# Kernel optimization log

Hardware: AMD Instinct MI355X
Metric: run time of the kernel (lower is better)

The kernel has to match this reference:

```python
import jax, jax.numpy as jnp
import numpy as np

E, D_IN, D_OUT = 8, 1024, 1024
B, S = 4, 2048

def setup_inputs() -> dict:
    key = jax.random.key(0)
    k_x, k_g, k_gb, k_w = jax.random.split(key, 4)
    x = jax.random.normal(k_x, (B, S, D_IN), dtype=jnp.float32)
    gate_w = jax.random.normal(k_g, (D_IN, E), dtype=jnp.float32) * 0.02
    gate_b = jax.random.normal(k_gb, (E,), dtype=jnp.float32) * 0.02
    expert_w = jax.random.normal(k_w, (E, D_IN, D_OUT), dtype=jnp.float32) * 0.02
    return {"x": x, "gate_w": gate_w, "gate_b": gate_b, "expert_w": expert_w}

def reference(x, gate_w, gate_b, expert_w):
    # gate: softmax over experts
    gate_score = jax.nn.softmax(x @ gate_w + gate_b, axis=-1)        # [B,S,E]
    # all-expert dense GEMM: [B,S,E,out]
    expert_out = jnp.einsum('bsi,eio->bseo', x, expert_w)
    # gate-weighted combine: [B,S,out]
    out = jnp.einsum('bse,bseo->bso', gate_score, expert_out)
    return out
```

## Files before the change

### kernel.cpp

```cpp
#include <hip/hip_runtime.h>
#include <hip/hip_bf16.h>
#include <cstdint>

#define TOKENS 8192
#define DIN 1024
#define DOUT 1024
#define NE 8

typedef __bf16 bf16;
typedef __attribute__((ext_vector_type(8))) __bf16 bf16x8;
typedef __attribute__((ext_vector_type(4))) float floatx4;
typedef __attribute__((ext_vector_type(2))) float floatx2;

__device__ __forceinline__ void async16(const void* gptr, void* lptr) {
  __builtin_amdgcn_global_load_lds(
      (const __attribute__((address_space(1))) void*)gptr,
      (__attribute__((address_space(3))) void*)lptr,
      16, 0, 0);
}

__global__ __launch_bounds__(256) void gate_kernel(
    const float* __restrict__ x, const float* __restrict__ gw,
    const float* __restrict__ gb, float* __restrict__ g,
    bf16* __restrict__ xbf) {
  __shared__ __align__(16) float gws[NE * DIN];
  __shared__ __align__(16) bf16 xtile[8][1032];

  const int tid = threadIdx.x;
  const int bg = blockIdx.x;
#pragma unroll
  for (int k = 0; k < 8; ++k) {
    const int base = (k * 256 + tid) * 4;
    const floatx4 v = *(const floatx4*)(gw + base);
#pragma unroll
    for (int m = 0; m < 4; ++m) {
      const int j = base + m;
      gws[(j & 7) * DIN + (j >> 3)] = v[m];
    }
  }
  __syncthreads();

  const int lane = tid & 63;
  const int wave = tid >> 6;

#pragma unroll
  for (int h = 0; h < 2; ++h) {
#pragma unroll
    for (int tt = 0; tt < 2; ++tt) {
      const int tl = h * 8 + tt * 4 + wave;
      const int t = bg * 16 + tl;
      const float* xr = x + (size_t)t * DIN;
      bf16* const xrow = &xtile[tl & 7][0];

      float acc[NE];
#pragma unroll
      for (int e = 0; e < NE; ++e) acc[e] = 0.f;

#pragma unroll
      for (int it = 0; it < 4; ++it) {
        const int i = it * 256 + lane * 4;
        const floatx4 xv = *(const floatx4*)(xr + i);
        union { bf16 b[4]; uint64_t u; } cv;
#pragma unroll
        for (int m = 0; m < 4; ++m) cv.b[m] = (bf16)xv[m];
        *(uint64_t*)(xrow + i) = cv.u;
#pragma unroll
        for (int e = 0; e < NE; ++e) {
          const floatx4 wv = *(const floatx4*)(gws + e * DIN + i);
          acc[e] += xv[0] * wv[0] + xv[1] * wv[1] + xv[2] * wv[2] + xv[3] * wv[3];
        }
      }
#pragma unroll
      for (int e = 0; e < NE; ++e)
#pragma unroll
        for (int off = 32; off > 0; off >>= 1)
          acc[e] += __shfl_xor(acc[e], off, 64);

      float lg[NE];
      float mx = -3.0e38f;
#pragma unroll
      for (int e = 0; e < NE; ++e) { lg[e] = acc[e] + gb[e]; mx = fmaxf(mx, lg[e]); }
      float s = 0.f;
#pragma unroll
      for (int e = 0; e < NE; ++e) { lg[e] = __expf(lg[e] - mx); s += lg[e]; }
      const float inv = 1.f / s;
      if (lane == 0) {
        floatx4 o0, o1;
#pragma unroll
        for (int e = 0; e < 4; ++e) { o0[e] = lg[e] * inv; o1[e] = lg[e + 4] * inv; }
        *(floatx4*)(g + (size_t)t * NE) = o0;
        *(floatx4*)(g + (size_t)t * NE + 4) = o1;
      }
    }
    __syncthreads();
#pragma unroll
    for (int p = 0; p < 4; ++p) {
      const int u = p * 256 + tid;
      const int lr3 = u & 7;
      const int lq = (u >> 3) & 3;
      const int kkv = (u >> 5) & 1;
      const int kt = u >> 6;
      const bf16x8 v = *(const bf16x8*)(&xtile[lr3][kt * 64 + kkv * 32 + lq * 8]);
      const size_t off = (size_t)bg * 16384 +
          (size_t)((((kt * 2 + kkv) * 4 + lq) * 16) + h * 8 + lr3) * 8;
      *(bf16x8*)(xbf + off) = v;
    }
    __syncthreads();
  }
}

__global__ __launch_bounds__(256) void trans_kernel(
    const float* __restrict__ w, bf16* __restrict__ wt) {
  __shared__ __align__(16) float tile[64][65];
  const int b = blockIdx.x;
  const int e = b >> 8;
  const int i0 = ((b >> 4) & 15) * 64;
  const int o0 = (b & 15) * 64;
  const int tid = threadIdx.x;
  const int c4 = (tid & 15) * 4;
  const int r = tid >> 4;

  const float* src = w + ((size_t)e * DIN + i0) * DOUT + o0;
#pragma unroll
  for (int rr = r; rr < 64; rr += 16) {
    const floatx4 v = *(const floatx4*)(src + (size_t)rr * DOUT + c4);
    tile[rr][c4] = v[0]; tile[rr][c4 + 1] = v[1];
    tile[rr][c4 + 2] = v[2]; tile[rr][c4 + 3] = v[3];
  }
  __syncthreads();
  bf16* dst = wt + ((size_t)e * DOUT + o0) * DIN + i0;
#pragma unroll
  for (int rr = r; rr < 64; rr += 16) {
    union { bf16 b[4]; uint64_t u; } cv;
#pragma unroll
    for (int j = 0; j < 4; ++j) cv.b[j] = (bf16)tile[c4 + j][rr];
    *(uint64_t*)(dst + (size_t)rr * DIN + c4) = cv.u;
  }
}

__global__ __launch_bounds__(256, 2) void moe_gemm(
    const bf16* __restrict__ xbf, const bf16* __restrict__ wt,
    const float* __restrict__ g, float* __restrict__ out) {
  __shared__ __align__(16) bf16 Bs[2][128 * 64];

  const int tid = threadIdx.x;
  const int c = blockIdx.x & 7;
  const int jj = blockIdx.x >> 3;
  const int bm = (c >> 1) * 16 + (jj & 15);
  const int bn = (c & 1) * 4 + (jj >> 4);
  const int lane = tid & 63;
  const int wave = tid >> 6;
  const int wm = wave >> 1, wn = wave & 1;
  const int lr = lane & 15, lq = lane >> 4;

  const int srow = tid >> 3;
  const int scol = (((tid & 7) ^ (srow & 7)) << 3);
  const int kx = lr & 7;

  const bf16* const bgp = wt + (size_t)(bn * 128 + srow) * DIN + scol;
  const bf16* const abase = xbf + (size_t)(bm * 8 + wm * 4) * 16384 + lane * 8;

  const floatx4 fzero = {0.f, 0.f, 0.f, 0.f};
  floatx4 accF[4][4], accE[4][4];
#pragma unroll
  for (int im = 0; im < 4; ++im)
#pragma unroll
    for (int in = 0; in < 4; ++in) { accF[im][in] = fzero; accE[im][in] = fzero; }

  const int tok0 = bm * 128 + wm * 64;

  {
    bf16* const blp = &Bs[0][tid * 8];
#pragma unroll
    for (int j = 0; j < 4; ++j)
      async16(bgp + (size_t)(32 * j) * DIN, blp + j * 2048);
  }
  bf16x8 avc[2][4], avn[2][4];
#pragma unroll
  for (int kk = 0; kk < 2; ++kk)
#pragma unroll
    for (int im = 0; im < 4; ++im)
      avc[kk][im] = *(const bf16x8*)(abase + (size_t)im * 16384 + kk * 512);
  __syncthreads();

  for (int t = 0; t < 128; ++t) {
    const bf16* const Bb = &Bs[t & 1][0];

    bf16x8 bv[2][4];
#pragma unroll
    for (int kk = 0; kk < 2; ++kk) {
      const int kg = ((kk * 4 + lq) ^ kx) << 3;
#pragma unroll
      for (int in = 0; in < 4; ++in)
        bv[kk][in] = *(const bf16x8*)(Bb + (wn * 64 + in * 16 + lr) * 64 + kg);
    }

    const int t1 = t + 1;
    if (t1 < 128) {
      const int kt1 = t1 & 15;
#pragma unroll
      for (int kk = 0; kk < 2; ++kk)
#pragma unroll
        for (int im = 0; im < 4; ++im)
          avn[kk][im] = *(const bf16x8*)(abase + (size_t)im * 16384 +
                                         (kt1 * 2 + kk) * 512);
      const bf16* const bsrc = bgp + ((size_t)(t1 >> 4) << 20) + (size_t)kt1 * 64;
      bf16* const blp = &Bs[t1 & 1][tid * 8];
#pragma unroll
      for (int j = 0; j < 4; ++j)
        async16(bsrc + (size_t)(32 * j) * DIN, blp + j * 2048);
    }

    __builtin_amdgcn_s_setprio(1);
#pragma unroll
    for (int im = 0; im < 4; ++im)
#pragma unroll
      for (int in = 0; in < 4; ++in)
        accE[im][in] = __builtin_amdgcn_mfma_f32_16x16x32_bf16(
            avc[0][im], bv[0][in], accE[im][in], 0, 0, 0);
    __builtin_amdgcn_s_setprio(0);

    __builtin_amdgcn_s_setprio(1);
#pragma unroll
    for (int im = 0; im < 4; ++im)
#pragma unroll
      for (int in = 0; in < 4; ++in)
        accE[im][in] = __builtin_amdgcn_mfma_f32_16x16x32_bf16(
            avc[1][im], bv[1][in], accE[im][in], 0, 0, 0);
    __builtin_amdgcn_s_setprio(0);

    if ((t & 15) == 15) {
      const int e = t >> 4;
#pragma unroll
      for (int im = 0; im < 4; ++im) {
        float gv[4];
#pragma unroll
        for (int r = 0; r < 4; ++r)
          gv[r] = g[(size_t)(tok0 + im * 16 + lq * 4 + r) * NE + e];
#pragma unroll
        for (int in = 0; in < 4; ++in)
#pragma unroll
          for (int r = 0; r < 4; ++r) {
            accF[im][in][r] += gv[r] * accE[im][in][r];
            accE[im][in][r] = 0.f;
          }
      }
    }

    __syncthreads();

#pragma unroll
    for (int kk = 0; kk < 2; ++kk)
#pragma unroll
      for (int im = 0; im < 4; ++im)
        avc[kk][im] = avn[kk][im];
  }

#pragma unroll
  for (int im = 0; im < 4; ++im)
#pragma unroll
    for (int in = 0; in < 4; ++in) {
      const int col = bn * 128 + wn * 64 + in * 16 + lr;
#pragma unroll
      for (int r = 0; r < 4; ++r)
        out[(size_t)(tok0 + im * 16 + lq * 4 + r) * DOUT + col] =
            accF[im][in][r];
    }
}

extern "C" void kernel_launch(void* const* d_in, const int* in_sizes, int n_in,
                              void* d_out, int out_size, void* d_ws,
                              size_t ws_size, hipStream_t stream) {
  const float* x  = (const float*)d_in[0];
  const float* gw = (const float*)d_in[1];
  const float* gb = (const float*)d_in[2];
  const float* w  = (const float*)d_in[3];
  float* out = (float*)d_out;

  char* ws = (char*)d_ws;
  float* g   = (float*)ws;
  bf16* xbf  = (bf16*)(ws + 262144);
  bf16* wt   = (bf16*)(ws + 262144 + (size_t)TOKENS * DIN * 2);

  trans_kernel<<<2048, 256, 0, stream>>>(w, wt);
  gate_kernel<<<512, 256, 0, stream>>>(x, gw, gb, g, xbf);
  moe_gemm<<<512, 256, 0, stream>>>(xbf, wt, g, out);
}
```

Baseline: 242.1 us.

## Merge prep kernels and deepen GEMM B-tile pipeline to four LDS stages

```diff
diff --git a/kernel.cpp b/kernel.cpp
--- a/kernel.cpp
+++ b/kernel.cpp
@@ -10,7 +10,6 @@
 typedef __bf16 bf16;
 typedef __attribute__((ext_vector_type(8))) __bf16 bf16x8;
 typedef __attribute__((ext_vector_type(4))) float floatx4;
-typedef __attribute__((ext_vector_type(2))) float floatx2;
 
 __device__ __forceinline__ void async16(const void* gptr, void* lptr) {
   __builtin_amdgcn_global_load_lds(
@@ -19,129 +18,201 @@
       16, 0, 0);
 }
 
-__global__ __launch_bounds__(256) void gate_kernel(
+__global__ __launch_bounds__(256) void prep_kernel(
     const float* __restrict__ x, const float* __restrict__ gw,
     const float* __restrict__ gb, float* __restrict__ g,
-    bf16* __restrict__ xbf) {
-  __shared__ __align__(16) float gws[NE * DIN];
+    bf16* __restrict__ xbf, const float* __restrict__ w,
+    bf16* __restrict__ wt) {
+  __shared__ __align__(16) float smem[NE * DIN];
   __shared__ __align__(16) bf16 xtile[8][1032];
 
   const int tid = threadIdx.x;
-  const int bg = blockIdx.x;
-#pragma unroll
-  for (int k = 0; k < 8; ++k) {
-    const int base = (k * 256 + tid) * 4;
-    const floatx4 v = *(const floatx4*)(gw + base);
-#pragma unroll
-    for (int m = 0; m < 4; ++m) {
-      const int j = base + m;
-      gws[(j & 7) * DIN + (j >> 3)] = v[m];
-    }
-  }
-  __syncthreads();
-
-  const int lane = tid & 63;
-  const int wave = tid >> 6;
-
-#pragma unroll
-  for (int h = 0; h < 2; ++h) {
-#pragma unroll
-    for (int tt = 0; tt < 2; ++tt) {
-      const int tl = h * 8 + tt * 4 + wave;
-      const int t = bg * 16 + tl;
-      const float* xr = x + (size_t)t * DIN;
-      bf16* const xrow = &xtile[tl & 7][0];
-
-      float acc[NE];
-#pragma unroll
-      for (int e = 0; e < NE; ++e) acc[e] = 0.f;
-
-#pragma unroll
-      for (int it = 0; it < 4; ++it) {
-        const int i = it * 256 + lane * 4;
-        const floatx4 xv = *(const floatx4*)(xr + i);
-        union { bf16 b[4]; uint64_t u; } cv;
-#pragma unroll
-        for (int m = 0; m < 4; ++m) cv.b[m] = (bf16)xv[m];
-        *(uint64_t*)(xrow + i) = cv.u;
-#pragma unroll
-        for (int e = 0; e < NE; ++e) {
-          const floatx4 wv = *(const floatx4*)(gws + e * DIN + i);
-          acc[e] += xv[0] * wv[0] + xv[1] * wv[1] + xv[2] * wv[2] + xv[3] * wv[3];
+  if (blockIdx.x < 512) {
+    const int bg = blockIdx.x;
+#pragma unroll
+    for (int k = 0; k < 8; ++k) {
+      const int base = (k * 256 + tid) * 4;
+      const floatx4 v = *(const floatx4*)(gw + base);
+#pragma unroll
+      for (int m = 0; m < 4; ++m) {
+        const int j = base + m;
+        smem[(j & 7) * DIN + (j >> 3)] = v[m];
+      }
+    }
+    __syncthreads();
+
+    const int lane = tid & 63;
+    const int wave = tid >> 6;
+
+#pragma unroll
+    for (int h = 0; h < 2; ++h) {
+#pragma unroll
+      for (int tt = 0; tt < 2; ++tt) {
+        const int tl = h * 8 + tt * 4 + wave;
+        const int t = bg * 16 + tl;
+        const float* xr = x + (size_t)t * DIN;
+        bf16* const xrow = &xtile[tl & 7][0];
+
+        float acc[NE];
+#pragma unroll
+        for (int e = 0; e < NE; ++e) acc[e] = 0.f;
+
+#pragma unroll
+        for (int it = 0; it < 4; ++it) {
+          const int i = it * 256 + lane * 4;
+          const floatx4 xv = *(const floatx4*)(xr + i);
+          union { bf16 b[4]; uint64_t u; } cv;
+#pragma unroll
+          for (int m = 0; m < 4; ++m) cv.b[m] = (bf16)xv[m];
+          *(uint64_t*)(xrow + i) = cv.u;
+#pragma unroll
+          for (int e = 0; e < NE; ++e) {
+            const floatx4 wv = *(const floatx4*)(smem + e * DIN + i);
+            acc[e] += xv[0] * wv[0] + xv[1] * wv[1] + xv[2] * wv[2] + xv[3] * wv[3];
+          }
+        }
+#pragma unroll
+        for (int e = 0; e < NE; ++e)
+#pragma unroll
+          for (int off = 32; off > 0; off >>= 1)
+            acc[e] += __shfl_xor(acc[e], off, 64);
+
+        float lg[NE];
+        float mx = -3.0e38f;
+#pragma unroll
+        for (int e = 0; e < NE; ++e) { lg[e] = acc[e] + gb[e]; mx = fmaxf(mx, lg[e]); }
+        float s = 0.f;
+#pragma unroll
+        for (int e = 0; e < NE; ++e) { lg[e] = __expf(lg[e] - mx); s += lg[e]; }
+        const float inv = 1.f / s;
+        if (lane == 0) {
+          floatx4 o0, o1;
+#pragma unroll
+          for (int e = 0; e < 4; ++e) { o0[e] = lg[e] * inv; o1[e] = lg[e + 4] * inv; }
+          *(floatx4*)(g + (size_t)t * NE) = o0;
+          *(floatx4*)(g + (size_t)t * NE + 4) = o1;
         }
       }
-#pragma unroll
-      for (int e = 0; e < NE; ++e)
-#pragma unroll
-        for (int off = 32; off > 0; off >>= 1)
-          acc[e] += __shfl_xor(acc[e], off, 64);
-
-      float lg[NE];
-      float mx = -3.0e38f;
-#pragma unroll
-      for (int e = 0; e < NE; ++e) { lg[e] = acc[e] + gb[e]; mx = fmaxf(mx, lg[e]); }
-      float s = 0.f;
-#pragma unroll
-      for (int e = 0; e < NE; ++e) { lg[e] = __expf(lg[e] - mx); s += lg[e]; }
-      const float inv = 1.f / s;
-      if (lane == 0) {
-        floatx4 o0, o1;
-#pragma unroll
-        for (int e = 0; e < 4; ++e) { o0[e] = lg[e] * inv; o1[e] = lg[e + 4] * inv; }
-        *(floatx4*)(g + (size_t)t * NE) = o0;
-        *(floatx4*)(g + (size_t)t * NE + 4) = o1;
+      __syncthreads();
+#pragma unroll
+      for (int p = 0; p < 4; ++p) {
+        const int u = p * 256 + tid;
+        const int lr3 = u & 7;
+        const int lq = (u >> 3) & 3;
+        const int kkv = (u >> 5) & 1;
+        const int kt = u >> 6;
+        const bf16x8 v = *(const bf16x8*)(&xtile[lr3][kt * 64 + kkv * 32 + lq * 8]);
+        const size_t off = (size_t)bg * 16384 +
+            (size_t)((((kt * 2 + kkv) * 4 + lq) * 16) + h * 8 + lr3) * 8;
+        *(bf16x8*)(xbf + off) = v;
       }
+      __syncthreads();
+    }
+  } else {
+    float (*tile)[65] = (float(*)[65])smem;
+    const int bt = blockIdx.x - 512;
+    const int e = bt & 7;
+    const int j = bt >> 3;
+    const int i0 = (j >> 4) * 64;
+    const int o0 = (j & 15) * 64;
+    const int c4 = (tid & 15) * 4;
+    const int r = tid >> 4;
+
+    const float* src = w + ((size_t)e * DIN + i0) * DOUT + o0;
+#pragma unroll
+    for (int rr = r; rr < 64; rr += 16) {
+      const floatx4 v = *(const floatx4*)(src + (size_t)rr * DOUT + c4);
+      tile[rr][c4] = v[0]; tile[rr][c4 + 1] = v[1];
+      tile[rr][c4 + 2] = v[2]; tile[rr][c4 + 3] = v[3];
     }
     __syncthreads();
-#pragma unroll
-    for (int p = 0; p < 4; ++p) {
-      const int u = p * 256 + tid;
-      const int lr3 = u & 7;
-      const int lq = (u >> 3) & 3;
-      const int kkv = (u >> 5) & 1;
-      const int kt = u >> 6;
-      const bf16x8 v = *(const bf16x8*)(&xtile[lr3][kt * 64 + kkv * 32 + lq * 8]);
-      const size_t off = (size_t)bg * 16384 +
-          (size_t)((((kt * 2 + kkv) * 4 + lq) * 16) + h * 8 + lr3) * 8;
-      *(bf16x8*)(xbf + off) = v;
-    }
-    __syncthreads();
-  }
-}
-
-__global__ __launch_bounds__(256) void trans_kernel(
-    const float* __restrict__ w, bf16* __restrict__ wt) {
-  __shared__ __align__(16) float tile[64][65];
-  const int b = blockIdx.x;
-  const int e = b >> 8;
-  const int i0 = ((b >> 4) & 15) * 64;
-  const int o0 = (b & 15) * 64;
-  const int tid = threadIdx.x;
-  const int c4 = (tid & 15) * 4;
-  const int r = tid >> 4;
-
-  const float* src = w + ((size_t)e * DIN + i0) * DOUT + o0;
-#pragma unroll
-  for (int rr = r; rr < 64; rr += 16) {
-    const floatx4 v = *(const floatx4*)(src + (size_t)rr * DOUT + c4);
-    tile[rr][c4] = v[0]; tile[rr][c4 + 1] = v[1];
-    tile[rr][c4 + 2] = v[2]; tile[rr][c4 + 3] = v[3];
-  }
-  __syncthreads();
-  bf16* dst = wt + ((size_t)e * DOUT + o0) * DIN + i0;
-#pragma unroll
-  for (int rr = r; rr < 64; rr += 16) {
-    union { bf16 b[4]; uint64_t u; } cv;
-#pragma unroll
-    for (int j = 0; j < 4; ++j) cv.b[j] = (bf16)tile[c4 + j][rr];
-    *(uint64_t*)(dst + (size_t)rr * DIN + c4) = cv.u;
+    bf16* dst = wt + ((size_t)e * DOUT + o0) * DIN + i0;
+#pragma unroll
+    for (int rr = r; rr < 64; rr += 16) {
+      union { bf16 b[4]; uint64_t u; } cv;
+#pragma unroll
+      for (int jj = 0; jj < 4; ++jj) cv.b[jj] = (bf16)tile[c4 + jj][rr];
+      *(uint64_t*)(dst + (size_t)rr * DIN + c4) = cv.u;
+    }
+  }
+}
+
+template <int TOFF>
+__device__ __forceinline__ void gemm_body(
+    int e, bf16* Bs, const bf16* abase, const bf16* bgp, const float* g,
+    bf16x8 (&avv)[2][2][4], float (&gcur)[4][4],
+    floatx4 (&accE)[4][4], floatx4 (&accF)[4][4],
+    int tid, int tok0, int lq, int kx, int wn, int lr) {
+  constexpr int PAR = TOFF & 1;
+  const int T = e * 16 + TOFF;
+
+  if (T + 1 < 128) {
+    const int ktn = (T + 1) & 15;
+#pragma unroll
+    for (int kk = 0; kk < 2; ++kk)
+#pragma unroll
+      for (int im = 0; im < 4; ++im)
+        avv[PAR ^ 1][kk][im] = *(const bf16x8*)(abase + (size_t)im * 16384 +
+                                                (ktn * 2 + kk) * 512);
+  }
+  if constexpr (TOFF == 1)
+    asm volatile("s_waitcnt vmcnt(28)" ::: "memory");
+  else
+    asm volatile("s_waitcnt vmcnt(12)" ::: "memory");
+  __builtin_amdgcn_s_barrier();
+  asm volatile("" ::: "memory");
+  if (T + 3 < 128) {
+    const int ts = T + 3;
+    const bf16* const bsrc =
+        bgp + ((size_t)(ts >> 4) << 20) + (size_t)(ts & 15) * 64;
+    bf16* const blp = Bs + ((TOFF + 3) & 3) * 8192 + tid * 8;
+#pragma unroll
+    for (int j = 0; j < 4; ++j)
+      async16(bsrc + (size_t)(32 * j) * DIN, blp + j * 2048);
+  }
+  if constexpr (TOFF == 0) {
+#pragma unroll
+    for (int im = 0; im < 4; ++im)
+#pragma unroll
+      for (int r = 0; r < 4; ++r)
+        gcur[im][r] = g[(size_t)(tok0 + im * 16 + lq * 4 + r) * NE + e];
+  }
+  const bf16* const Bb = Bs + (TOFF & 3) * 8192;
+  bf16x8 bv[2][4];
+#pragma unroll
+  for (int kk = 0; kk < 2; ++kk) {
+    const int kg = ((kk * 4 + lq) ^ kx) << 3;
+#pragma unroll
+    for (int in = 0; in < 4; ++in)
+      bv[kk][in] = *(const bf16x8*)(Bb + (wn * 64 + in * 16 + lr) * 64 + kg);
+  }
+  __builtin_amdgcn_s_setprio(1);
+#pragma unroll
+  for (int kk = 0; kk < 2; ++kk)
+#pragma unroll
+    for (int im = 0; im < 4; ++im)
+#pragma unroll
+      for (int in = 0; in < 4; ++in)
+        accE[im][in] = __builtin_amdgcn_mfma_f32_16x16x32_bf16(
+            avv[PAR][kk][im], bv[kk][in], accE[im][in], 0, 0, 0);
+  __builtin_amdgcn_s_setprio(0);
+  if constexpr (TOFF == 15) {
+#pragma unroll
+    for (int im = 0; im < 4; ++im)
+#pragma unroll
+      for (int in = 0; in < 4; ++in)
+#pragma unroll
+        for (int r = 0; r < 4; ++r) {
+          accF[im][in][r] += gcur[im][r] * accE[im][in][r];
+          accE[im][in][r] = 0.f;
+        }
   }
 }
 
 __global__ __launch_bounds__(256, 2) void moe_gemm(
     const bf16* __restrict__ xbf, const bf16* __restrict__ wt,
     const float* __restrict__ g, float* __restrict__ out) {
-  __shared__ __align__(16) bf16 Bs[2][128 * 64];
+  __shared__ __align__(16) bf16 Bs[4 * 128 * 64];
 
   const int tid = threadIdx.x;
   const int c = blockIdx.x & 7;
@@ -169,91 +240,40 @@
 
   const int tok0 = bm * 128 + wm * 64;
 
-  {
-    bf16* const blp = &Bs[0][tid * 8];
+  bf16x8 avv[2][2][4];
+  float gcur[4][4];
+
+#pragma unroll
+  for (int s = 0; s < 3; ++s) {
+    const bf16* const bsrc = bgp + (size_t)s * 64;
+    bf16* const blp = Bs + s * 8192 + tid * 8;
 #pragma unroll
     for (int j = 0; j < 4; ++j)
-      async16(bgp + (size_t)(32 * j) * DIN, blp + j * 2048);
-  }
-  bf16x8 avc[2][4], avn[2][4];
+      async16(bsrc + (size_t)(32 * j) * DIN, blp + j * 2048);
+  }
 #pragma unroll
   for (int kk = 0; kk < 2; ++kk)
 #pragma unroll
     for (int im = 0; im < 4; ++im)
-      avc[kk][im] = *(const bf16x8*)(abase + (size_t)im * 16384 + kk * 512);
-  __syncthreads();
-
-  for (int t = 0; t < 128; ++t) {
-    const bf16* const Bb = &Bs[t & 1][0];
-
-    bf16x8 bv[2][4];
-#pragma unroll
-    for (int kk = 0; kk < 2; ++kk) {
-      const int kg = ((kk * 4 + lq) ^ kx) << 3;
-#pragma unroll
-      for (int in = 0; in < 4; ++in)
-        bv[kk][in] = *(const bf16x8*)(Bb + (wn * 64 + in * 16 + lr) * 64 + kg);
-    }
-
-    const int t1 = t + 1;
-    if (t1 < 128) {
-      const int kt1 = t1 & 15;
-#pragma unroll
-      for (int kk = 0; kk < 2; ++kk)
-#pragma unroll
-        for (int im = 0; im < 4; ++im)
-          avn[kk][im] = *(const bf16x8*)(abase + (size_t)im * 16384 +
-                                         (kt1 * 2 + kk) * 512);
-      const bf16* const bsrc = bgp + ((size_t)(t1 >> 4) << 20) + (size_t)kt1 * 64;
-      bf16* const blp = &Bs[t1 & 1][tid * 8];
-#pragma unroll
-      for (int j = 0; j < 4; ++j)
-        async16(bsrc + (size_t)(32 * j) * DIN, blp + j * 2048);
-    }
-
-    __builtin_amdgcn_s_setprio(1);
-#pragma unroll
-    for (int im = 0; im < 4; ++im)
-#pragma unroll
-      for (int in = 0; in < 4; ++in)
-        accE[im][in] = __builtin_amdgcn_mfma_f32_16x16x32_bf16(
-            avc[0][im], bv[0][in], accE[im][in], 0, 0, 0);
-    __builtin_amdgcn_s_setprio(0);
-
-    __builtin_amdgcn_s_setprio(1);
-#pragma unroll
-    for (int im = 0; im < 4; ++im)
-#pragma unroll
-      for (int in = 0; in < 4; ++in)
-        accE[im][in] = __builtin_amdgcn_mfma_f32_16x16x32_bf16(
-            avc[1][im], bv[1][in], accE[im][in], 0, 0, 0);
-    __builtin_amdgcn_s_setprio(0);
-
-    if ((t & 15) == 15) {
-      const int e = t >> 4;
-#pragma unroll
-      for (int im = 0; im < 4; ++im) {
-        float gv[4];
-#pragma unroll
-        for (int r = 0; r < 4; ++r)
-          gv[r] = g[(size_t)(tok0 + im * 16 + lq * 4 + r) * NE + e];
-#pragma unroll
-        for (int in = 0; in < 4; ++in)
-#pragma unroll
-          for (int r = 0; r < 4; ++r) {
-            accF[im][in][r] += gv[r] * accE[im][in][r];
-            accE[im][in][r] = 0.f;
-          }
-      }
-    }
-
-    __syncthreads();
-
-#pragma unroll
-    for (int kk = 0; kk < 2; ++kk)
-#pragma unroll
-      for (int im = 0; im < 4; ++im)
-        avc[kk][im] = avn[kk][im];
+      avv[0][kk][im] = *(const bf16x8*)(abase + (size_t)im * 16384 + kk * 512);
+
+  for (int e = 0; e < NE; ++e) {
+    gemm_body<0>(e, Bs, abase, bgp, g, avv, gcur, accE, accF, tid, tok0, lq, kx, wn, lr);
+    gemm_body<1>(e, Bs, abase, bgp, g, avv, gcur, accE, accF, tid, tok0, lq, kx, wn, lr);
+    gemm_body<2>(e, Bs, abase, bgp, g, avv, gcur, accE, accF, tid, tok0, lq, kx, wn, lr);
+    gemm_body<3>(e, Bs, abase, bgp, g, avv, gcur, accE, accF, tid, tok0, lq, kx, wn, lr);
+    gemm_body<4>(e, Bs, abase, bgp, g, avv, gcur, accE, accF, tid, tok0, lq, kx, wn, lr);
+    gemm_body<5>(e, Bs, abase, bgp, g, avv, gcur, accE, accF, tid, tok0, lq, kx, wn, lr);
+    gemm_body<6>(e, Bs, abase, bgp, g, avv, gcur, accE, accF, tid, tok0, lq, kx, wn, lr);
+    gemm_body<7>(e, Bs, abase, bgp, g, avv, gcur, accE, accF, tid, tok0, lq, kx, wn, lr);
+    gemm_body<8>(e, Bs, abase, bgp, g, avv, gcur, accE, accF, tid, tok0, lq, kx, wn, lr);
+    gemm_body<9>(e, Bs, abase, bgp, g, avv, gcur, accE, accF, tid, tok0, lq, kx, wn, lr);
+    gemm_body<10>(e, Bs, abase, bgp, g, avv, gcur, accE, accF, tid, tok0, lq, kx, wn, lr);
+    gemm_body<11>(e, Bs, abase, bgp, g, avv, gcur, accE, accF, tid, tok0, lq, kx, wn, lr);
+    gemm_body<12>(e, Bs, abase, bgp, g, avv, gcur, accE, accF, tid, tok0, lq, kx, wn, lr);
+    gemm_body<13>(e, Bs, abase, bgp, g, avv, gcur, accE, accF, tid, tok0, lq, kx, wn, lr);
+    gemm_body<14>(e, Bs, abase, bgp, g, avv, gcur, accE, accF, tid, tok0, lq, kx, wn, lr);
+    gemm_body<15>(e, Bs, abase, bgp, g, avv, gcur, accE, accF, tid, tok0, lq, kx, wn, lr);
   }
 
 #pragma unroll
@@ -282,7 +302,6 @@
   bf16* xbf  = (bf16*)(ws + 262144);
   bf16* wt   = (bf16*)(ws + 262144 + (size_t)TOKENS * DIN * 2);
 
-  trans_kernel<<<2048, 256, 0, stream>>>(w, wt);
-  gate_kernel<<<512, 256, 0, stream>>>(x, gw, gb, g, xbf);
+  prep_kernel<<<2560, 256, 0, stream>>>(x, gw, gb, g, xbf, w, wt);
   moe_gemm<<<512, 256, 0, stream>>>(xbf, wt, g, out);
 }
```

New measurement: 663.8 us. 2.74x slower.
